# Kernel tuning notes

Hardware: AMD Instinct MI355X
Metric: run time of the kernel (lower is better)

Reference implementation:

```python
import jax, jax.numpy as jnp
import numpy as np

HEADS = 16
NUM_CHUNKS = 8  # min(int(log2(4096))+1, 8)


def setup_inputs() -> dict:
    key = jax.random.key(0)
    ks = jax.random.split(key, 6)
    B, T, C = 4, 4096, 1024
    s = 1.0 / np.sqrt(C)
    x = jax.random.normal(ks[0], (B, T, C), jnp.float32)
    Wqkv = jax.random.normal(ks[1], (3 * C, C), jnp.float32) * s
    Wout = jax.random.normal(ks[2], (C, C), jnp.float32) * s
    bout = jnp.zeros((C,), jnp.float32)
    Wl1 = jax.random.normal(ks[3], (64, 1), jnp.float32)
    bl1 = jnp.zeros((64,), jnp.float32)
    Wl2 = jax.random.normal(ks[4], (HEADS, 64), jnp.float32) * 0.125
    bl2 = jnp.zeros((HEADS,), jnp.float32)
    return dict(x=x, Wqkv=Wqkv, Wout=Wout, bout=bout, Wl1=Wl1, bl1=bl1, Wl2=Wl2, bl2=bl2)


def reference(x, Wqkv, Wout, bout, Wl1, bl1, Wl2, bl2):
    B, T, C = x.shape
    H = HEADS
    dh = C // H
    nc = NUM_CHUNKS
    cs = T // nc
    scale = dh ** (-0.5)

    # qkv projection (torch Linear: x @ W.T), split, to [B,H,T,dh]
    qkv = x @ Wqkv.T  # [B,T,3C]
    q, k, v = jnp.split(qkv, 3, axis=-1)
    def heads(t):
        return t.reshape(B, T, H, dh).transpose(0, 2, 1, 3)
    q, k, v = heads(q), heads(k), heads(v)

    # lambda gates from log positions: [T,1] -> [T,H] -> [H,T]
    log_pos = jnp.log(jnp.arange(T, dtype=jnp.float32) + 1.0)[:, None]
    h1 = jax.nn.relu(log_pos @ Wl1.T + bl1)            # [T,64]
    lam = jax.nn.sigmoid(h1 @ Wl2.T + bl2).T           # [H,T]
    lam = lam.reshape(H, nc, cs)                        # per-chunk key gates

    # block-local (chunked) attention, fully vectorized over chunks
    qc = q.reshape(B, H, nc, cs, dh)
    kc = k.reshape(B, H, nc, cs, dh)
    vc = v.reshape(B, H, nc, cs, dh)
    scores = jnp.einsum('bhnqd,bhnkd->bhnqk', qc, kc) * scale
    scores = scores * lam[None, :, :, None, :]          # gate keys pre-softmax
    attn = jax.nn.softmax(scores, axis=-1)
    out = jnp.einsum('bhnqk,bhnkd->bhnqd', attn, vc)    # [B,H,nc,cs,dh]

    out = out.reshape(B, H, T, dh).transpose(0, 2, 1, 3).reshape(B, T, C)
    return out @ Wout.T + bout
```

## Files before the change

kernel.cpp:

```cpp
#include <hip/hip_runtime.h>
#include <hip/hip_bf16.h>

typedef unsigned short u16;
typedef __attribute__((ext_vector_type(8))) short v8s;
typedef __attribute__((ext_vector_type(4))) float v4f;
typedef __attribute__((ext_vector_type(16))) float v16f;
typedef __attribute__((ext_vector_type(4))) unsigned v4u;

#define DEV __device__ __forceinline__

DEV u16 f2bf(float f) {
  union { float f; unsigned u; } v; v.f = f;
  unsigned r = v.u + 0x7fffu + ((v.u >> 16) & 1u);
  return (u16)(r >> 16);
}

DEV unsigned pk2bf(float a, float b) {
  float2 t; t.x = a; t.y = b;
  __hip_bfloat162 p = __float22bfloat162_rn(t);
  union { __hip_bfloat162 h; unsigned u; } c; c.h = p;
  return c.u;
}

DEV void gload_lds16(const void* g, void* l) {
  __builtin_amdgcn_global_load_lds(
      (const __attribute__((address_space(1))) void*)g,
      (__attribute__((address_space(3))) void*)l, 16, 0, 0);
}

__global__ __launch_bounds__(256) void cvt_bf16(const float* __restrict__ in,
                                                u16* __restrict__ out, int n4) {
  int i = blockIdx.x * 256 + threadIdx.x;
  if (i >= n4) return;
  float4 v = ((const float4*)in)[i];
  ushort4 o;
  o.x = f2bf(v.x); o.y = f2bf(v.y); o.z = f2bf(v.z); o.w = f2bf(v.w);
  ((ushort4*)out)[i] = o;
}

__global__ __launch_bounds__(256) void lam_kernel(const float* __restrict__ Wl1,
    const float* __restrict__ bl1, const float* __restrict__ Wl2,
    const float* __restrict__ bl2, float* __restrict__ lam) {
  int t = blockIdx.x * 256 + threadIdx.x;
  float lp = logf((float)t + 1.0f);
  float h1[64];
#pragma unroll
  for (int j = 0; j < 64; ++j) h1[j] = fmaxf(lp * Wl1[j] + bl1[j], 0.0f);
#pragma unroll 1
  for (int h = 0; h < 16; ++h) {
    float z = bl2[h];
#pragma unroll
    for (int j = 0; j < 64; ++j) z += h1[j] * Wl2[h * 64 + j];
    lam[h * 4096 + t] = 0.125f / (1.0f + expf(-z));
  }
}

template <int MH>
DEV void mfma32(v4f (&acc)[8][4], const v8s (&a)[4][2], const v8s (&b)[4][2]) {
#pragma unroll
  for (int kk = 0; kk < 2; ++kk)
#pragma unroll
    for (int i = 0; i < 4; ++i)
#pragma unroll
      for (int j = 0; j < 4; ++j)
        acc[MH * 4 + i][j] = __builtin_amdgcn_mfma_f32_16x16x32_bf16(
            a[i][kk], b[j][kk], acc[MH * 4 + i][j], 0, 0, 0);
}

DEV void ldA(v8s (&a)[4][2], const u16* Ab, int wr, int mh, int lane) {
  const int l15 = lane & 15, g = lane >> 4;
#pragma unroll
  for (int i = 0; i < 4; ++i) {
    const int row = wr * 128 + mh * 64 + i * 16 + l15;
#pragma unroll
    for (int kk = 0; kk < 2; ++kk)
      a[i][kk] = *(const v8s*)(Ab + row * 64 + (((kk * 4 + g) ^ (row & 7)) << 3));
  }
}

DEV void ldB4(v8s (&b)[4][2], const u16* Bb, int wc, int lane) {
  const int l15 = lane & 15, g = lane >> 4;
#pragma unroll
  for (int j = 0; j < 4; ++j) {
    const int row = (j >> 1) * 128 + wc * 32 + (j & 1) * 16 + l15;
#pragma unroll
    for (int kk = 0; kk < 2; ++kk)
      b[j][kk] = *(const v8s*)(Bb + row * 64 + (((kk * 4 + g) ^ (row & 7)) << 3));
  }
}

template <int OUTF32>
__global__ __launch_bounds__(512, 2) void gemm256(const u16* __restrict__ A,
    const u16* __restrict__ Bt, void* __restrict__ Cout,
    const float* __restrict__ bias, int M, int N, int K) {
  __shared__ u16 As[2][256 * 64];
  __shared__ u16 Bs[2][256 * 64];
  const int tid = threadIdx.x;
  const int lane = tid & 63;
  const int nbn = N >> 8;
  const int nwg = gridDim.x;
  int wg = blockIdx.x;
  wg = (wg & 7) * (nwg >> 3) + (wg >> 3);
  const int m0 = (wg / nbn) << 8;
  const int n0 = (wg % nbn) << 8;
  const int wid = tid >> 6;
  const int wr = wid >> 2;
  const int wc = wid & 3;
  const int nkt = K >> 6;
  const int nit = nkt >> 1;

  auto SAu = [&](int buf, int kt, int u) {
    const int ur = tid >> 3;
    const int slot = (tid & 7) ^ (ur & 7);
    gload_lds16(A + (size_t)(m0 + u * 64 + ur) * K + kt * 64 + slot * 8,
                &As[buf][u * 4096 + (tid & ~63) * 8]);
  };
  auto SBu = [&](int buf, int kt, int u) {
    const int q = tid >> 3;
    const int grow = (((u & 1) * 2 + (q >> 5)) << 6) + ((u >> 1) << 5) + (q & 31);
    const int slot = (tid & 7) ^ (q & 7);
    gload_lds16(Bt + (size_t)(n0 + grow) * K + kt * 64 + slot * 8,
                &Bs[buf][u * 4096 + (tid & ~63) * 8]);
  };
  auto SA_ = [&](int buf, int kt, int mh) { SAu(buf, kt, mh); SAu(buf, kt, 2 + mh); };
  auto SB_ = [&](int buf, int kt, int nh) { SBu(buf, kt, nh * 2); SBu(buf, kt, nh * 2 + 1); };

  v4f acc[8][4] = {};
  v8s a[4][2], b[4][2];

  SA_(0, 0, 0); SA_(0, 0, 1); SB_(0, 0, 0); SB_(0, 0, 1);
  SA_(1, 1, 0); SB_(1, 1, 0); SB_(1, 1, 1);
  asm volatile("s_waitcnt vmcnt(6)" ::: "memory");
  asm volatile("s_barrier" ::: "memory");

#define PHASE(MHc, VM, ...)                                 \
  do { __VA_ARGS__; } while (0);                            \
  __builtin_amdgcn_s_setprio(1);                            \
  mfma32<MHc>(acc, a, b);                                   \
  __builtin_amdgcn_s_setprio(0);                            \
  if (VM) asm volatile("s_waitcnt vmcnt(6)" ::: "memory");  \
  asm volatile("s_barrier" ::: "memory");

  for (int it = 0; it < nit; ++it) {
    const int t0 = 2 * it;
    const int t1 = t0 + 1;
    const int t2 = (t0 + 2 < nkt) ? t0 + 2 : nkt - 1;
    const int t3 = (t0 + 3 < nkt) ? t0 + 3 : nkt - 1;
    ldA(a, As[0], wr, 0, lane); ldB4(b, Bs[0], wc, lane);
    PHASE(0, 0, SAu(1, t1, 1); SAu(1, t1, 3));
    ldA(a, As[0], wr, 1, lane);
    PHASE(1, 1, SB_(0, t2, 0); SB_(0, t2, 1); SAu(0, t2, 0); SAu(0, t2, 2));
    ldA(a, As[1], wr, 0, lane); ldB4(b, Bs[1], wc, lane);
    PHASE(0, 0, SAu(0, t2, 1); SAu(0, t2, 3));
    ldA(a, As[1], wr, 1, lane);
    PHASE(1, 1, SB_(1, t3, 0); SB_(1, t3, 1); SAu(1, t3, 0); SAu(1, t3, 2));
  }
#undef PHASE

  const int l15 = lane & 15, g4 = (lane >> 4) * 4;
#pragma unroll
  for (int i = 0; i < 8; ++i) {
#pragma unroll
    for (int j = 0; j < 4; ++j) {
      const int gr = m0 + wr * 128 + i * 16 + g4;
      const int gc = n0 + wc * 64 + j * 16 + l15;
      float bv = OUTF32 ? bias[gc] : 0.0f;
#pragma unroll
      for (int r = 0; r < 4; ++r) {
        float val = acc[i][j][r];
        if (OUTF32) ((float*)Cout)[(size_t)(gr + r) * N + gc] = val + bv;
        else ((u16*)Cout)[(size_t)(gr + r) * N + gc] = f2bf(val);
      }
    }
  }
}

__global__ __launch_bounds__(512) void attn_chunk(const u16* __restrict__ qkv,
    const float* __restrict__ lam, u16* __restrict__ aout) {
  __shared__ u16 Ksm[512 * 64];
  __shared__ u16 Vt[64 * 520];
  __shared__ float lam_s[512];

  const int tid = threadIdx.x;
  const int lane = tid & 63;
  const int wid = tid >> 6;
  const int blk = blockIdx.x;
  const int c = blk & 7;
  const int hd = (blk >> 3) & 15;
  const int b = blk >> 7;
  const size_t tok0 = (size_t)b * 4096 + c * 512;
  const u16* qb = qkv + tok0 * 3072 + hd * 64;
  const u16* kb = qb + 1024;
  const u16* vb = qb + 2048;

  lam_s[tid] = lam[hd * 4096 + c * 512 + tid];

#pragma unroll
  for (int i = 0; i < 8; ++i) {
    const int r = i * 64 + wid * 8 + (lane >> 3);
    const int f = (r & 3) | (((r >> 3) & 1) << 2);
    gload_lds16(kb + (size_t)r * 3072 + (((lane & 7) ^ f) << 3),
                &Ksm[(i * 64 + wid * 8) * 64]);
  }
  {
    const int pr = tid & 255;
    const int k0 = 2 * pr;
    const int kg = k0 & 31;
    const int col = (k0 & ~31) + (kg & 16) + (((kg >> 2) & 1) << 3) +
                    ((kg & 3) | ((kg & 8) >> 1));
    const int db0 = (tid >> 8) * 4;
#pragma unroll
    for (int dbi = 0; dbi < 4; ++dbi) {
      const int d0 = (db0 + dbi) * 8;
      v8s v0 = *(const v8s*)(vb + (size_t)k0 * 3072 + d0);
      v8s v1 = *(const v8s*)(vb + (size_t)(k0 + 1) * 3072 + d0);
#pragma unroll
      for (int j = 0; j < 8; ++j) {
        unsigned pk = (unsigned)(u16)v0[j] | ((unsigned)(u16)v1[j] << 16);
        *(unsigned*)&Vt[(d0 + j) * 520 + col] = pk;
      }
    }
  }
  __syncthreads();

  const int l31 = lane & 31;
  const int hf = lane >> 5;
  const int fk = (l31 & 3) | (((l31 >> 3) & 1) << 2);

#pragma unroll 1
  for (int pass = 0; pass < 2; ++pass) {
    const int q0 = pass * 256 + wid * 32;
    v8s qv[4];
#pragma unroll
    for (int dsec = 0; dsec < 4; ++dsec)
      qv[dsec] = *(const v8s*)(qb + (size_t)(q0 + l31) * 3072 + dsec * 16 + hf * 8);

    float m = -1e30f, sum = 0.0f;
    v16f o0 = {}, o1 = {};

#pragma unroll 1
    for (int kt = 0; kt < 16; ++kt) {
      v16f acc = {};
#pragma unroll
      for (int dsec = 0; dsec < 4; ++dsec) {
        const v8s kf = *(const v8s*)&Ksm[(kt * 32 + l31) * 64 +
                                         (((dsec * 2 + hf) ^ fk) << 3)];
        acc = __builtin_amdgcn_mfma_f32_32x32x16_bf16(kf, qv[dsec], acc, 0, 0, 0);
      }
#pragma unroll
      for (int a = 0; a < 4; ++a) {
        const v4f lv = *(const v4f*)&lam_s[kt * 32 + a * 8 + hf * 4];
#pragma unroll
        for (int i = 0; i < 4; ++i) acc[4 * a + i] *= lv[i];
      }
      float tm = acc[0];
#pragma unroll
      for (int r = 1; r < 16; ++r) tm = fmaxf(tm, acc[r]);
      tm = fmaxf(tm, __shfl_xor(tm, 32));
      if (!__all(tm <= m + 8.0f)) {
        const float nm = fmaxf(m, tm);
        const float sc = __expf(m - nm);
        sum *= sc;
        o0 *= sc; o1 *= sc;
        m = nm;
      }
      float ps = 0.0f;
#pragma unroll
      for (int r = 0; r < 16; ++r) { acc[r] = __expf(acc[r] - m); ps += acc[r]; }
      sum += ps;
      v4u pa, pb;
      pa.x = pk2bf(acc[0], acc[1]);   pa.y = pk2bf(acc[2], acc[3]);
      pa.z = pk2bf(acc[4], acc[5]);   pa.w = pk2bf(acc[6], acc[7]);
      pb.x = pk2bf(acc[8], acc[9]);   pb.y = pk2bf(acc[10], acc[11]);
      pb.z = pk2bf(acc[12], acc[13]); pb.w = pk2bf(acc[14], acc[15]);
      const v8s pfA = __builtin_bit_cast(v8s, pa);
      const v8s pfB = __builtin_bit_cast(v8s, pb);
      const int vcol = kt * 32 + hf * 8;
      const v8s vA0 = *(const v8s*)&Vt[l31 * 520 + vcol];
      const v8s vB0 = *(const v8s*)&Vt[l31 * 520 + vcol + 16];
      const v8s vA1 = *(const v8s*)&Vt[(32 + l31) * 520 + vcol];
      const v8s vB1 = *(const v8s*)&Vt[(32 + l31) * 520 + vcol + 16];
      o0 = __builtin_amdgcn_mfma_f32_32x32x16_bf16(vA0, pfA, o0, 0, 0, 0);
      o0 = __builtin_amdgcn_mfma_f32_32x32x16_bf16(vB0, pfB, o0, 0, 0, 0);
      o1 = __builtin_amdgcn_mfma_f32_32x32x16_bf16(vA1, pfA, o1, 0, 0, 0);
      o1 = __builtin_amdgcn_mfma_f32_32x32x16_bf16(vB1, pfB, o1, 0, 0, 0);
    }

    sum += __shfl_xor(sum, 32);
    const float sv = 1.0f / sum;

    const size_t obase = (tok0 + q0 + l31) * 1024 + hd * 64;
#pragma unroll
    for (int a = 0; a < 4; ++a) {
      ushort4 w0, w1;
      w0.x = f2bf(o0[4 * a + 0] * sv); w0.y = f2bf(o0[4 * a + 1] * sv);
      w0.z = f2bf(o0[4 * a + 2] * sv); w0.w = f2bf(o0[4 * a + 3] * sv);
      w1.x = f2bf(o1[4 * a + 0] * sv); w1.y = f2bf(o1[4 * a + 1] * sv);
      w1.z = f2bf(o1[4 * a + 2] * sv); w1.w = f2bf(o1[4 * a + 3] * sv);
      *(ushort4*)&aout[obase + 8 * a + 4 * hf] = w0;
      *(ushort4*)&aout[obase + 32 + 8 * a + 4 * hf] = w1;
    }
  }
}

extern "C" void kernel_launch(void* const* d_in, const int* in_sizes, int n_in,
                              void* d_out, int out_size, void* d_ws, size_t ws_size,
                              hipStream_t stream) {
  const float* x    = (const float*)d_in[0];
  const float* Wqkv = (const float*)d_in[1];
  const float* Wout = (const float*)d_in[2];
  const float* bout = (const float*)d_in[3];
  const float* Wl1  = (const float*)d_in[4];
  const float* bl1  = (const float*)d_in[5];
  const float* Wl2  = (const float*)d_in[6];
  const float* bl2  = (const float*)d_in[7];
  float* out = (float*)d_out;

  char* ws = (char*)d_ws;
  u16* xbf    = (u16*)ws; ws += (size_t)16384 * 1024 * 2;
  u16* wqkvbf = (u16*)ws; ws += (size_t)3072 * 1024 * 2;
  u16* woutbf = (u16*)ws; ws += (size_t)1024 * 1024 * 2;
  u16* qkvbf  = (u16*)ws; ws += (size_t)16384 * 3072 * 2;
  u16* aoutbf = (u16*)ws; ws += (size_t)16384 * 1024 * 2;
  float* lam  = (float*)ws; ws += (size_t)16 * 4096 * 4;

  cvt_bf16<<<16384, 256, 0, stream>>>(x, xbf, 16777216 / 4);
  cvt_bf16<<<3072, 256, 0, stream>>>(Wqkv, wqkvbf, 3145728 / 4);
  cvt_bf16<<<1024, 256, 0, stream>>>(Wout, woutbf, 1048576 / 4);
  lam_kernel<<<16, 256, 0, stream>>>(Wl1, bl1, Wl2, bl2, lam);

  gemm256<0><<<dim3((16384 / 256) * (3072 / 256)), 512, 0, stream>>>(
      xbf, wqkvbf, qkvbf, nullptr, 16384, 3072, 1024);

  attn_chunk<<<512, 512, 0, stream>>>(qkvbf, lam, aoutbf);

  gemm256<1><<<dim3((16384 / 256) * (1024 / 256)), 512, 0, stream>>>(
      aoutbf, woutbf, out, bout, 16384, 1024, 1024);
}
```

Before: 248.4 us.

## Use 1024-thread attention blocks and double-buffer A fragments in GEMM

The attention kernel now launches 1024 threads per block, so each of 16 waves handles one 32-query tile in a single pass instead of two passes of 8 waves. The K/V staging loops are halved to match. Separately, the GEMM main loop loads both A fragment halves into distinct registers (a0/a1) up front, so the second LDS read no longer sits between the MFMA phases. This raises register pressure in the GEMM and, through the launch bounds of 1024 threads, caps registers per thread in the attention kernel, which may cause spills.

```diff
diff --git a/kernel.cpp b/kernel.cpp
--- a/kernel.cpp
+++ b/kernel.cpp
@@ -126,17 +126,17 @@
   auto SB_ = [&](int buf, int kt, int nh) { SBu(buf, kt, nh * 2); SBu(buf, kt, nh * 2 + 1); };
 
   v4f acc[8][4] = {};
-  v8s a[4][2], b[4][2];
+  v8s a0[4][2], a1[4][2], b[4][2];
 
   SA_(0, 0, 0); SA_(0, 0, 1); SB_(0, 0, 0); SB_(0, 0, 1);
   SA_(1, 1, 0); SB_(1, 1, 0); SB_(1, 1, 1);
   asm volatile("s_waitcnt vmcnt(6)" ::: "memory");
   asm volatile("s_barrier" ::: "memory");
 
-#define PHASE(MHc, VM, ...)                                 \
+#define PHASE(MHc, AREG, VM, ...)                           \
   do { __VA_ARGS__; } while (0);                            \
   __builtin_amdgcn_s_setprio(1);                            \
-  mfma32<MHc>(acc, a, b);                                   \
+  mfma32<MHc>(acc, AREG, b);                                \
   __builtin_amdgcn_s_setprio(0);                            \
   if (VM) asm volatile("s_waitcnt vmcnt(6)" ::: "memory");  \
   asm volatile("s_barrier" ::: "memory");
@@ -146,14 +146,14 @@
     const int t1 = t0 + 1;
     const int t2 = (t0 + 2 < nkt) ? t0 + 2 : nkt - 1;
     const int t3 = (t0 + 3 < nkt) ? t0 + 3 : nkt - 1;
-    ldA(a, As[0], wr, 0, lane); ldB4(b, Bs[0], wc, lane);
-    PHASE(0, 0, SAu(1, t1, 1); SAu(1, t1, 3));
-    ldA(a, As[0], wr, 1, lane);
-    PHASE(1, 1, SB_(0, t2, 0); SB_(0, t2, 1); SAu(0, t2, 0); SAu(0, t2, 2));
-    ldA(a, As[1], wr, 0, lane); ldB4(b, Bs[1], wc, lane);
-    PHASE(0, 0, SAu(0, t2, 1); SAu(0, t2, 3));
-    ldA(a, As[1], wr, 1, lane);
-    PHASE(1, 1, SB_(1, t3, 0); SB_(1, t3, 1); SAu(1, t3, 0); SAu(1, t3, 2));
+    ldA(a0, As[0], wr, 0, lane); ldB4(b, Bs[0], wc, lane);
+    ldA(a1, As[0], wr, 1, lane);
+    PHASE(0, a0, 0, SAu(1, t1, 1); SAu(1, t1, 3));
+    PHASE(1, a1, 1, SB_(0, t2, 0); SB_(0, t2, 1); SAu(0, t2, 0); SAu(0, t2, 2));
+    ldA(a0, As[1], wr, 0, lane); ldB4(b, Bs[1], wc, lane);
+    ldA(a1, As[1], wr, 1, lane);
+    PHASE(0, a0, 0, SAu(0, t2, 1); SAu(0, t2, 3));
+    PHASE(1, a1, 1, SB_(1, t3, 0); SB_(1, t3, 1); SAu(1, t3, 0); SAu(1, t3, 2));
   }
 #undef PHASE
 
@@ -175,7 +175,7 @@
   }
 }
 
-__global__ __launch_bounds__(512) void attn_chunk(const u16* __restrict__ qkv,
+__global__ __launch_bounds__(1024, 4) void attn_chunk(const u16* __restrict__ qkv,
     const float* __restrict__ lam, u16* __restrict__ aout) {
   __shared__ u16 Ksm[512 * 64];
   __shared__ u16 Vt[64 * 520];
@@ -193,14 +193,14 @@
   const u16* kb = qb + 1024;
   const u16* vb = qb + 2048;
 
-  lam_s[tid] = lam[hd * 4096 + c * 512 + tid];
-
-#pragma unroll
-  for (int i = 0; i < 8; ++i) {
-    const int r = i * 64 + wid * 8 + (lane >> 3);
+  if (tid < 512) lam_s[tid] = lam[hd * 4096 + c * 512 + tid];
+
+#pragma unroll
+  for (int i = 0; i < 4; ++i) {
+    const int r = i * 128 + wid * 8 + (lane >> 3);
     const int f = (r & 3) | (((r >> 3) & 1) << 2);
     gload_lds16(kb + (size_t)r * 3072 + (((lane & 7) ^ f) << 3),
-                &Ksm[(i * 64 + wid * 8) * 64]);
+                &Ksm[(i * 128 + wid * 8) * 64]);
   }
   {
     const int pr = tid & 255;
@@ -208,9 +208,9 @@
     const int kg = k0 & 31;
     const int col = (k0 & ~31) + (kg & 16) + (((kg >> 2) & 1) << 3) +
                     ((kg & 3) | ((kg & 8) >> 1));
-    const int db0 = (tid >> 8) * 4;
-#pragma unroll
-    for (int dbi = 0; dbi < 4; ++dbi) {
+    const int db0 = (tid >> 8) * 2;
+#pragma unroll
+    for (int dbi = 0; dbi < 2; ++dbi) {
       const int d0 = (db0 + dbi) * 8;
       v8s v0 = *(const v8s*)(vb + (size_t)k0 * 3072 + d0);
       v8s v1 = *(const v8s*)(vb + (size_t)(k0 + 1) * 3072 + d0);
@@ -227,79 +227,76 @@
   const int hf = lane >> 5;
   const int fk = (l31 & 3) | (((l31 >> 3) & 1) << 2);
 
+  const int q0 = wid * 32;
+  v8s qv[4];
+#pragma unroll
+  for (int dsec = 0; dsec < 4; ++dsec)
+    qv[dsec] = *(const v8s*)(qb + (size_t)(q0 + l31) * 3072 + dsec * 16 + hf * 8);
+
+  float m = -1e30f, sum = 0.0f;
+  v16f o0 = {}, o1 = {};
+
 #pragma unroll 1
-  for (int pass = 0; pass < 2; ++pass) {
-    const int q0 = pass * 256 + wid * 32;
-    v8s qv[4];
-#pragma unroll
-    for (int dsec = 0; dsec < 4; ++dsec)
-      qv[dsec] = *(const v8s*)(qb + (size_t)(q0 + l31) * 3072 + dsec * 16 + hf * 8);
-
-    float m = -1e30f, sum = 0.0f;
-    v16f o0 = {}, o1 = {};
-
-#pragma unroll 1
-    for (int kt = 0; kt < 16; ++kt) {
-      v16f acc = {};
-#pragma unroll
-      for (int dsec = 0; dsec < 4; ++dsec) {
-        const v8s kf = *(const v8s*)&Ksm[(kt * 32 + l31) * 64 +
-                                         (((dsec * 2 + hf) ^ fk) << 3)];
-        acc = __builtin_amdgcn_mfma_f32_32x32x16_bf16(kf, qv[dsec], acc, 0, 0, 0);
-      }
-#pragma unroll
-      for (int a = 0; a < 4; ++a) {
-        const v4f lv = *(const v4f*)&lam_s[kt * 32 + a * 8 + hf * 4];
-#pragma unroll
-        for (int i = 0; i < 4; ++i) acc[4 * a + i] *= lv[i];
-      }
-      float tm = acc[0];
-#pragma unroll
-      for (int r = 1; r < 16; ++r) tm = fmaxf(tm, acc[r]);
-      tm = fmaxf(tm, __shfl_xor(tm, 32));
-      if (!__all(tm <= m + 8.0f)) {
-        const float nm = fmaxf(m, tm);
-        const float sc = __expf(m - nm);
-        sum *= sc;
-        o0 *= sc; o1 *= sc;
-        m = nm;
-      }
-      float ps = 0.0f;
-#pragma unroll
-      for (int r = 0; r < 16; ++r) { acc[r] = __expf(acc[r] - m); ps += acc[r]; }
-      sum += ps;
-      v4u pa, pb;
-      pa.x = pk2bf(acc[0], acc[1]);   pa.y = pk2bf(acc[2], acc[3]);
-      pa.z = pk2bf(acc[4], acc[5]);   pa.w = pk2bf(acc[6], acc[7]);
-      pb.x = pk2bf(acc[8], acc[9]);   pb.y = pk2bf(acc[10], acc[11]);
-      pb.z = pk2bf(acc[12], acc[13]); pb.w = pk2bf(acc[14], acc[15]);
-      const v8s pfA = __builtin_bit_cast(v8s, pa);
-      const v8s pfB = __builtin_bit_cast(v8s, pb);
-      const int vcol = kt * 32 + hf * 8;
-      const v8s vA0 = *(const v8s*)&Vt[l31 * 520 + vcol];
-      const v8s vB0 = *(const v8s*)&Vt[l31 * 520 + vcol + 16];
-      const v8s vA1 = *(const v8s*)&Vt[(32 + l31) * 520 + vcol];
-      const v8s vB1 = *(const v8s*)&Vt[(32 + l31) * 520 + vcol + 16];
-      o0 = __builtin_amdgcn_mfma_f32_32x32x16_bf16(vA0, pfA, o0, 0, 0, 0);
-      o0 = __builtin_amdgcn_mfma_f32_32x32x16_bf16(vB0, pfB, o0, 0, 0, 0);
-      o1 = __builtin_amdgcn_mfma_f32_32x32x16_bf16(vA1, pfA, o1, 0, 0, 0);
-      o1 = __builtin_amdgcn_mfma_f32_32x32x16_bf16(vB1, pfB, o1, 0, 0, 0);
-    }
-
-    sum += __shfl_xor(sum, 32);
-    const float sv = 1.0f / sum;
-
-    const size_t obase = (tok0 + q0 + l31) * 1024 + hd * 64;
+  for (int kt = 0; kt < 16; ++kt) {
+    v16f acc = {};
+#pragma unroll
+    for (int dsec = 0; dsec < 4; ++dsec) {
+      const v8s kf = *(const v8s*)&Ksm[(kt * 32 + l31) * 64 +
+                                       (((dsec * 2 + hf) ^ fk) << 3)];
+      acc = __builtin_amdgcn_mfma_f32_32x32x16_bf16(kf, qv[dsec], acc, 0, 0, 0);
+    }
 #pragma unroll
     for (int a = 0; a < 4; ++a) {
-      ushort4 w0, w1;
-      w0.x = f2bf(o0[4 * a + 0] * sv); w0.y = f2bf(o0[4 * a + 1] * sv);
-      w0.z = f2bf(o0[4 * a + 2] * sv); w0.w = f2bf(o0[4 * a + 3] * sv);
-      w1.x = f2bf(o1[4 * a + 0] * sv); w1.y = f2bf(o1[4 * a + 1] * sv);
-      w1.z = f2bf(o1[4 * a + 2] * sv); w1.w = f2bf(o1[4 * a + 3] * sv);
-      *(ushort4*)&aout[obase + 8 * a + 4 * hf] = w0;
-      *(ushort4*)&aout[obase + 32 + 8 * a + 4 * hf] = w1;
-    }
+      const v4f lv = *(const v4f*)&lam_s[kt * 32 + a * 8 + hf * 4];
+#pragma unroll
+      for (int i = 0; i < 4; ++i) acc[4 * a + i] *= lv[i];
+    }
+    float tm = acc[0];
+#pragma unroll
+    for (int r = 1; r < 16; ++r) tm = fmaxf(tm, acc[r]);
+    tm = fmaxf(tm, __shfl_xor(tm, 32));
+    if (!__all(tm <= m + 8.0f)) {
+      const float nm = fmaxf(m, tm);
+      const float sc = __expf(m - nm);
+      sum *= sc;
+      o0 *= sc; o1 *= sc;
+      m = nm;
+    }
+    float ps = 0.0f;
+#pragma unroll
+    for (int r = 0; r < 16; ++r) { acc[r] = __expf(acc[r] - m); ps += acc[r]; }
+    sum += ps;
+    v4u pa, pb;
+    pa.x = pk2bf(acc[0], acc[1]);   pa.y = pk2bf(acc[2], acc[3]);
+    pa.z = pk2bf(acc[4], acc[5]);   pa.w = pk2bf(acc[6], acc[7]);
+    pb.x = pk2bf(acc[8], acc[9]);   pb.y = pk2bf(acc[10], acc[11]);
+    pb.z = pk2bf(acc[12], acc[13]); pb.w = pk2bf(acc[14], acc[15]);
+    const v8s pfA = __builtin_bit_cast(v8s, pa);
+    const v8s pfB = __builtin_bit_cast(v8s, pb);
+    const int vcol = kt * 32 + hf * 8;
+    const v8s vA0 = *(const v8s*)&Vt[l31 * 520 + vcol];
+    const v8s vB0 = *(const v8s*)&Vt[l31 * 520 + vcol + 16];
+    const v8s vA1 = *(const v8s*)&Vt[(32 + l31) * 520 + vcol];
+    const v8s vB1 = *(const v8s*)&Vt[(32 + l31) * 520 + vcol + 16];
+    o0 = __builtin_amdgcn_mfma_f32_32x32x16_bf16(vA0, pfA, o0, 0, 0, 0);
+    o0 = __builtin_amdgcn_mfma_f32_32x32x16_bf16(vB0, pfB, o0, 0, 0, 0);
+    o1 = __builtin_amdgcn_mfma_f32_32x32x16_bf16(vA1, pfA, o1, 0, 0, 0);
+    o1 = __builtin_amdgcn_mfma_f32_32x32x16_bf16(vB1, pfB, o1, 0, 0, 0);
+  }
+
+  sum += __shfl_xor(sum, 32);
+  const float sv = 1.0f / sum;
+
+  const size_t obase = (tok0 + q0 + l31) * 1024 + hd * 64;
+#pragma unroll
+  for (int a = 0; a < 4; ++a) {
+    ushort4 w0, w1;
+    w0.x = f2bf(o0[4 * a + 0] * sv); w0.y = f2bf(o0[4 * a + 1] * sv);
+    w0.z = f2bf(o0[4 * a + 2] * sv); w0.w = f2bf(o0[4 * a + 3] * sv);
+    w1.x = f2bf(o1[4 * a + 0] * sv); w1.y = f2bf(o1[4 * a + 1] * sv);
+    w1.z = f2bf(o1[4 * a + 2] * sv); w1.w = f2bf(o1[4 * a + 3] * sv);
+    *(ushort4*)&aout[obase + 8 * a + 4 * hf] = w0;
+    *(ushort4*)&aout[obase + 32 + 8 * a + 4 * hf] = w1;
   }
 }
 
@@ -332,7 +329,7 @@
   gemm256<0><<<dim3((16384 / 256) * (3072 / 256)), 512, 0, stream>>>(
       xbf, wqkvbf, qkvbf, nullptr, 16384, 3072, 1024);
 
-  attn_chunk<<<512, 512, 0, stream>>>(qkvbf, lam, aoutbf);
+  attn_chunk<<<512, 1024, 0, stream>>>(qkvbf, lam, aoutbf);
 
   gemm256<1><<<dim3((16384 / 256) * (1024 / 256)), 512, 0, stream>>>(
       aoutbf, woutbf, out, bout, 16384, 1024, 1024);
```

New measurement: 244.7 us. About the same (-1.5%).

## Swap GEMM MFMA operands for vectorized stores; use 1024-thread attention blocks

Applied to the files above, without the earlier changes.

In the GEMM, the MFMA A/B operands are swapped so each lane holds four consecutive output columns. That lets the epilogue write float4/ushort4 vectors instead of scalar strided stores. The attention kernel moves from 512 threads doing two query passes to 1024 threads (16 waves) each handling one 32-query tile, with the K/V staging loops split across the extra threads. This aims to raise parallelism and latency hiding in attention, but the larger block raises register pressure under the new launch bounds.

```diff
diff --git a/kernel.cpp b/kernel.cpp
--- a/kernel.cpp
+++ b/kernel.cpp
@@ -64,7 +64,7 @@
 #pragma unroll
       for (int j = 0; j < 4; ++j)
         acc[MH * 4 + i][j] = __builtin_amdgcn_mfma_f32_16x16x32_bf16(
-            a[i][kk], b[j][kk], acc[MH * 4 + i][j], 0, 0, 0);
+            b[j][kk], a[i][kk], acc[MH * 4 + i][j], 0, 0, 0);
 }
 
 DEV void ldA(v8s (&a)[4][2], const u16* Ab, int wr, int mh, int lane) {
@@ -162,20 +162,25 @@
   for (int i = 0; i < 8; ++i) {
 #pragma unroll
     for (int j = 0; j < 4; ++j) {
-      const int gr = m0 + wr * 128 + i * 16 + g4;
-      const int gc = n0 + wc * 64 + j * 16 + l15;
-      float bv = OUTF32 ? bias[gc] : 0.0f;
-#pragma unroll
-      for (int r = 0; r < 4; ++r) {
-        float val = acc[i][j][r];
-        if (OUTF32) ((float*)Cout)[(size_t)(gr + r) * N + gc] = val + bv;
-        else ((u16*)Cout)[(size_t)(gr + r) * N + gc] = f2bf(val);
+      const int gm = m0 + wr * 128 + i * 16 + l15;
+      const int gn = n0 + wc * 64 + j * 16 + g4;
+      if (OUTF32) {
+        const float4 bv = *(const float4*)&bias[gn];
+        float4 w;
+        w.x = acc[i][j][0] + bv.x; w.y = acc[i][j][1] + bv.y;
+        w.z = acc[i][j][2] + bv.z; w.w = acc[i][j][3] + bv.w;
+        *(float4*)&((float*)Cout)[(size_t)gm * N + gn] = w;
+      } else {
+        ushort4 w;
+        w.x = f2bf(acc[i][j][0]); w.y = f2bf(acc[i][j][1]);
+        w.z = f2bf(acc[i][j][2]); w.w = f2bf(acc[i][j][3]);
+        *(ushort4*)&((u16*)Cout)[(size_t)gm * N + gn] = w;
       }
     }
   }
 }
 
-__global__ __launch_bounds__(512) void attn_chunk(const u16* __restrict__ qkv,
+__global__ __launch_bounds__(1024, 4) void attn_chunk(const u16* __restrict__ qkv,
     const float* __restrict__ lam, u16* __restrict__ aout) {
   __shared__ u16 Ksm[512 * 64];
   __shared__ u16 Vt[64 * 520];
@@ -193,14 +198,14 @@
   const u16* kb = qb + 1024;
   const u16* vb = qb + 2048;
 
-  lam_s[tid] = lam[hd * 4096 + c * 512 + tid];
-
-#pragma unroll
-  for (int i = 0; i < 8; ++i) {
-    const int r = i * 64 + wid * 8 + (lane >> 3);
+  if (tid < 512) lam_s[tid] = lam[hd * 4096 + c * 512 + tid];
+
+#pragma unroll
+  for (int i = 0; i < 4; ++i) {
+    const int r = i * 128 + wid * 8 + (lane >> 3);
     const int f = (r & 3) | (((r >> 3) & 1) << 2);
     gload_lds16(kb + (size_t)r * 3072 + (((lane & 7) ^ f) << 3),
-                &Ksm[(i * 64 + wid * 8) * 64]);
+                &Ksm[(i * 128 + wid * 8) * 64]);
   }
   {
     const int pr = tid & 255;
@@ -208,9 +213,9 @@
     const int kg = k0 & 31;
     const int col = (k0 & ~31) + (kg & 16) + (((kg >> 2) & 1) << 3) +
                     ((kg & 3) | ((kg & 8) >> 1));
-    const int db0 = (tid >> 8) * 4;
-#pragma unroll
-    for (int dbi = 0; dbi < 4; ++dbi) {
+    const int db0 = (tid >> 8) * 2;
+#pragma unroll
+    for (int dbi = 0; dbi < 2; ++dbi) {
       const int d0 = (db0 + dbi) * 8;
       v8s v0 = *(const v8s*)(vb + (size_t)k0 * 3072 + d0);
       v8s v1 = *(const v8s*)(vb + (size_t)(k0 + 1) * 3072 + d0);
@@ -227,79 +232,76 @@
   const int hf = lane >> 5;
   const int fk = (l31 & 3) | (((l31 >> 3) & 1) << 2);
 
+  const int q0 = wid * 32;
+  v8s qv[4];
+#pragma unroll
+  for (int dsec = 0; dsec < 4; ++dsec)
+    qv[dsec] = *(const v8s*)(qb + (size_t)(q0 + l31) * 3072 + dsec * 16 + hf * 8);
+
+  float m = -1e30f, sum = 0.0f;
+  v16f o0 = {}, o1 = {};
+
 #pragma unroll 1
-  for (int pass = 0; pass < 2; ++pass) {
-    const int q0 = pass * 256 + wid * 32;
-    v8s qv[4];
-#pragma unroll
-    for (int dsec = 0; dsec < 4; ++dsec)
-      qv[dsec] = *(const v8s*)(qb + (size_t)(q0 + l31) * 3072 + dsec * 16 + hf * 8);
-
-    float m = -1e30f, sum = 0.0f;
-    v16f o0 = {}, o1 = {};
-
-#pragma unroll 1
-    for (int kt = 0; kt < 16; ++kt) {
-      v16f acc = {};
-#pragma unroll
-      for (int dsec = 0; dsec < 4; ++dsec) {
-        const v8s kf = *(const v8s*)&Ksm[(kt * 32 + l31) * 64 +
-                                         (((dsec * 2 + hf) ^ fk) << 3)];
-        acc = __builtin_amdgcn_mfma_f32_32x32x16_bf16(kf, qv[dsec], acc, 0, 0, 0);
-      }
-#pragma unroll
-      for (int a = 0; a < 4; ++a) {
-        const v4f lv = *(const v4f*)&lam_s[kt * 32 + a * 8 + hf * 4];
-#pragma unroll
-        for (int i = 0; i < 4; ++i) acc[4 * a + i] *= lv[i];
-      }
-      float tm = acc[0];
-#pragma unroll
-      for (int r = 1; r < 16; ++r) tm = fmaxf(tm, acc[r]);
-      tm = fmaxf(tm, __shfl_xor(tm, 32));
-      if (!__all(tm <= m + 8.0f)) {
-        const float nm = fmaxf(m, tm);
-        const float sc = __expf(m - nm);
-        sum *= sc;
-        o0 *= sc; o1 *= sc;
-        m = nm;
-      }
-      float ps = 0.0f;
-#pragma unroll
-      for (int r = 0; r < 16; ++r) { acc[r] = __expf(acc[r] - m); ps += acc[r]; }
-      sum += ps;
-      v4u pa, pb;
-      pa.x = pk2bf(acc[0], acc[1]);   pa.y = pk2bf(acc[2], acc[3]);
-      pa.z = pk2bf(acc[4], acc[5]);   pa.w = pk2bf(acc[6], acc[7]);
-      pb.x = pk2bf(acc[8], acc[9]);   pb.y = pk2bf(acc[10], acc[11]);
-      pb.z = pk2bf(acc[12], acc[13]); pb.w = pk2bf(acc[14], acc[15]);
-      const v8s pfA = __builtin_bit_cast(v8s, pa);
-      const v8s pfB = __builtin_bit_cast(v8s, pb);
-      const int vcol = kt * 32 + hf * 8;
-      const v8s vA0 = *(const v8s*)&Vt[l31 * 520 + vcol];
-      const v8s vB0 = *(const v8s*)&Vt[l31 * 520 + vcol + 16];
-      const v8s vA1 = *(const v8s*)&Vt[(32 + l31) * 520 + vcol];
-      const v8s vB1 = *(const v8s*)&Vt[(32 + l31) * 520 + vcol + 16];
-      o0 = __builtin_amdgcn_mfma_f32_32x32x16_bf16(vA0, pfA, o0, 0, 0, 0);
-      o0 = __builtin_amdgcn_mfma_f32_32x32x16_bf16(vB0, pfB, o0, 0, 0, 0);
-      o1 = __builtin_amdgcn_mfma_f32_32x32x16_bf16(vA1, pfA, o1, 0, 0, 0);
-      o1 = __builtin_amdgcn_mfma_f32_32x32x16_bf16(vB1, pfB, o1, 0, 0, 0);
-    }
-
-    sum += __shfl_xor(sum, 32);
-    const float sv = 1.0f / sum;
-
-    const size_t obase = (tok0 + q0 + l31) * 1024 + hd * 64;
+  for (int kt = 0; kt < 16; ++kt) {
+    v16f acc = {};
+#pragma unroll
+    for (int dsec = 0; dsec < 4; ++dsec) {
+      const v8s kf = *(const v8s*)&Ksm[(kt * 32 + l31) * 64 +
+                                       (((dsec * 2 + hf) ^ fk) << 3)];
+      acc = __builtin_amdgcn_mfma_f32_32x32x16_bf16(kf, qv[dsec], acc, 0, 0, 0);
+    }
 #pragma unroll
     for (int a = 0; a < 4; ++a) {
-      ushort4 w0, w1;
-      w0.x = f2bf(o0[4 * a + 0] * sv); w0.y = f2bf(o0[4 * a + 1] * sv);
-      w0.z = f2bf(o0[4 * a + 2] * sv); w0.w = f2bf(o0[4 * a + 3] * sv);
-      w1.x = f2bf(o1[4 * a + 0] * sv); w1.y = f2bf(o1[4 * a + 1] * sv);
-      w1.z = f2bf(o1[4 * a + 2] * sv); w1.w = f2bf(o1[4 * a + 3] * sv);
-      *(ushort4*)&aout[obase + 8 * a + 4 * hf] = w0;
-      *(ushort4*)&aout[obase + 32 + 8 * a + 4 * hf] = w1;
-    }
+      const v4f lv = *(const v4f*)&lam_s[kt * 32 + a * 8 + hf * 4];
+#pragma unroll
+      for (int i = 0; i < 4; ++i) acc[4 * a + i] *= lv[i];
+    }
+    float tm = acc[0];
+#pragma unroll
+    for (int r = 1; r < 16; ++r) tm = fmaxf(tm, acc[r]);
+    tm = fmaxf(tm, __shfl_xor(tm, 32));
+    if (!__all(tm <= m + 8.0f)) {
+      const float nm = fmaxf(m, tm);
+      const float sc = __expf(m - nm);
+      sum *= sc;
+      o0 *= sc; o1 *= sc;
+      m = nm;
+    }
+    float ps = 0.0f;
+#pragma unroll
+    for (int r = 0; r < 16; ++r) { acc[r] = __expf(acc[r] - m); ps += acc[r]; }
+    sum += ps;
+    v4u pa, pb;
+    pa.x = pk2bf(acc[0], acc[1]);   pa.y = pk2bf(acc[2], acc[3]);
+    pa.z = pk2bf(acc[4], acc[5]);   pa.w = pk2bf(acc[6], acc[7]);
+    pb.x = pk2bf(acc[8], acc[9]);   pb.y = pk2bf(acc[10], acc[11]);
+    pb.z = pk2bf(acc[12], acc[13]); pb.w = pk2bf(acc[14], acc[15]);
+    const v8s pfA = __builtin_bit_cast(v8s, pa);
+    const v8s pfB = __builtin_bit_cast(v8s, pb);
+    const int vcol = kt * 32 + hf * 8;
+    const v8s vA0 = *(const v8s*)&Vt[l31 * 520 + vcol];
+    const v8s vB0 = *(const v8s*)&Vt[l31 * 520 + vcol + 16];
+    const v8s vA1 = *(const v8s*)&Vt[(32 + l31) * 520 + vcol];
+    const v8s vB1 = *(const v8s*)&Vt[(32 + l31) * 520 + vcol + 16];
+    o0 = __builtin_amdgcn_mfma_f32_32x32x16_bf16(vA0, pfA, o0, 0, 0, 0);
+    o0 = __builtin_amdgcn_mfma_f32_32x32x16_bf16(vB0, pfB, o0, 0, 0, 0);
+    o1 = __builtin_amdgcn_mfma_f32_32x32x16_bf16(vA1, pfA, o1, 0, 0, 0);
+    o1 = __builtin_amdgcn_mfma_f32_32x32x16_bf16(vB1, pfB, o1, 0, 0, 0);
+  }
+
+  sum += __shfl_xor(sum, 32);
+  const float sv = 1.0f / sum;
+
+  const size_t obase = (tok0 + q0 + l31) * 1024 + hd * 64;
+#pragma unroll
+  for (int a = 0; a < 4; ++a) {
+    ushort4 w0, w1;
+    w0.x = f2bf(o0[4 * a + 0] * sv); w0.y = f2bf(o0[4 * a + 1] * sv);
+    w0.z = f2bf(o0[4 * a + 2] * sv); w0.w = f2bf(o0[4 * a + 3] * sv);
+    w1.x = f2bf(o1[4 * a + 0] * sv); w1.y = f2bf(o1[4 * a + 1] * sv);
+    w1.z = f2bf(o1[4 * a + 2] * sv); w1.w = f2bf(o1[4 * a + 3] * sv);
+    *(ushort4*)&aout[obase + 8 * a + 4 * hf] = w0;
+    *(ushort4*)&aout[obase + 32 + 8 * a + 4 * hf] = w1;
   }
 }
 
@@ -332,7 +334,7 @@
   gemm256<0><<<dim3((16384 / 256) * (3072 / 256)), 512, 0, stream>>>(
       xbf, wqkvbf, qkvbf, nullptr, 16384, 3072, 1024);
 
-  attn_chunk<<<512, 512, 0, stream>>>(qkvbf, lam, aoutbf);
+  attn_chunk<<<512, 1024, 0, stream>>>(qkvbf, lam, aoutbf);
 
   gemm256<1><<<dim3((16384 / 256) * (1024 / 256)), 512, 0, stream>>>(
       aoutbf, woutbf, out, bout, 16384, 1024, 1024);
```

Measured after the change: 258.4 us (median of 4 runs). +4.0%, slower.
